# Performance work log

Hardware: AMD Instinct MI355X
Metric: run time of the kernel (lower is better)

## Reference

```python
import jax, jax.numpy as jnp
import numpy as np

D = 512
H = 8
DK = D // H
FF = 4 * D
EPS = 1e-5
NEG = -1.0e9


def _layernorm(x, g, b):
    mu = jnp.mean(x, axis=-1, keepdims=True)
    var = jnp.mean((x - mu) ** 2, axis=-1, keepdims=True)
    return (x - mu) * jax.lax.rsqrt(var + EPS) * g + b


def setup_inputs() -> dict:
    key = jax.random.key(0)
    ks = jax.random.split(key, 16)
    B, S = 4, 2048
    x = jax.random.normal(ks[0], (B, S, D), dtype=jnp.float32)
    # causal mask, broadcastable to [B, H, S, S]; mask==0 -> blocked
    mask = jnp.tril(jnp.ones((S, S), dtype=jnp.int32))[None, None]
    s = 1.0 / np.sqrt(D)
    sf = 1.0 / np.sqrt(FF)
    p = {
        "wq": jax.random.normal(ks[1], (D, D), jnp.float32) * s,
        "bq": jnp.zeros((D,), jnp.float32),
        "wk": jax.random.normal(ks[2], (D, D), jnp.float32) * s,
        "bk": jnp.zeros((D,), jnp.float32),
        "wv": jax.random.normal(ks[3], (D, D), jnp.float32) * s,
        "bv": jnp.zeros((D,), jnp.float32),
        "wo": jax.random.normal(ks[4], (D, D), jnp.float32) * s,
        "bo": jnp.zeros((D,), jnp.float32),
        "w1": jax.random.normal(ks[5], (D, FF), jnp.float32) * s,
        "b1": jnp.zeros((FF,), jnp.float32),
        "w2": jax.random.normal(ks[6], (FF, D), jnp.float32) * sf,
        "b2": jnp.zeros((D,), jnp.float32),
        "g1": jnp.ones((D,), jnp.float32),
        "be1": jnp.zeros((D,), jnp.float32),
        "g2": jnp.ones((D,), jnp.float32),
        "be2": jnp.zeros((D,), jnp.float32),
    }
    return {"x": x, "mask": mask, **p}


def reference(x, mask, wq, bq, wk, bk, wv, bv, wo, bo, w1, b1, w2, b2, g1, be1, g2, be2):
    B, S, _ = x.shape
    # projections -> [B, H, S, DK]
    q = (x @ wq + bq).reshape(B, S, H, DK).transpose(0, 2, 1, 3)
    k = (x @ wk + bk).reshape(B, S, H, DK).transpose(0, 2, 1, 3)
    v = (x @ wv + bv).reshape(B, S, H, DK).transpose(0, 2, 1, 3)
    scores = jnp.einsum("bhqd,bhkd->bhqk", q, k) / np.sqrt(DK)
    scores = jnp.where(mask == 0, NEG, scores)
    attn = jax.nn.softmax(scores, axis=-1)
    ctx = jnp.einsum("bhqk,bhkd->bhqd", attn, v)
    ctx = ctx.transpose(0, 2, 1, 3).reshape(B, S, D)
    attn_out = ctx @ wo + bo
    # dropout is inference-mode identity
    h = _layernorm(x + attn_out, g1, be1)
    ffn = jax.nn.relu(h @ w1 + b1) @ w2 + b2
    return _layernorm(h + ffn, g2, be2)
```

## Files before the change

kernel.cpp:

```cpp
#include <hip/hip_runtime.h>
#include <math.h>

#define D_   512
#define H_   8
#define DK_  64
#define FF_  2048
#define S_   2048
#define B_   4
#define M_   (B_*S_)
#define EPS_ 1e-5f
#define SCLQ 0.1803368801111f

typedef __attribute__((ext_vector_type(8))) short bf16x8;
typedef __attribute__((ext_vector_type(4))) float f32x4;
typedef __attribute__((ext_vector_type(4))) unsigned int u32x4;

__device__ inline unsigned short f2b(float f) {
    unsigned u = __builtin_bit_cast(unsigned, f);
    unsigned r = (u + 0x7FFFu + ((u >> 16) & 1u)) >> 16;
    return (unsigned short)r;
}
__device__ inline float b2f(unsigned short u) {
    return __builtin_bit_cast(float, (unsigned)u << 16);
}
__device__ inline unsigned packbf(float p0, float p1) {
    unsigned r;
    asm("v_cvt_pk_bf16_f32 %0, %1, %2" : "=v"(r) : "v"(p0), "v"(p1));
    return r;
}

__device__ __forceinline__ void async_cp16(const void* g, void* l) {
    __builtin_amdgcn_global_load_lds(
        (const __attribute__((address_space(1))) unsigned int*)g,
        (__attribute__((address_space(3))) unsigned int*)l, 16, 0, 0);
}

__global__ __launch_bounds__(256)
void prep_kernel(const float* __restrict__ x,
                 const float* __restrict__ wq, const float* __restrict__ wk,
                 const float* __restrict__ wv, const float* __restrict__ wo,
                 const float* __restrict__ bq, const float* __restrict__ bk,
                 const float* __restrict__ bv,
                 const float* __restrict__ w1, const float* __restrict__ w2,
                 unsigned short* __restrict__ xb, unsigned short* __restrict__ wqkvt,
                 unsigned short* __restrict__ wot, unsigned short* __restrict__ w1t,
                 unsigned short* __restrict__ w2t, float* __restrict__ bqkv)
{
    __shared__ float L[32][33];
    const int bid = blockIdx.x;
    const int tid = threadIdx.x;

    if (bid < 2048) {
        const int i = (bid * 256 + tid) * 8;
        const float4 a = *(const float4*)(x + i);
        const float4 b = *(const float4*)(x + i + 4);
        bf16x8 v;
        v[0] = (short)f2b(a.x); v[1] = (short)f2b(a.y);
        v[2] = (short)f2b(a.z); v[3] = (short)f2b(a.w);
        v[4] = (short)f2b(b.x); v[5] = (short)f2b(b.y);
        v[6] = (short)f2b(b.z); v[7] = (short)f2b(b.w);
        *(bf16x8*)(xb + i) = v;
        return;
    }

    const float* w; unsigned short* wt; int K, N, k0, n0; float scl = 1.f;
    if (bid < 3072) {
        const int z = (bid - 2048) >> 8;
        const int r = (bid - 2048) & 255;
        n0 = (r & 15) * 32; k0 = (r >> 4) * 32; K = 512; N = 512;
        w  = (z == 0) ? wq : (z == 1) ? wk : (z == 2) ? wv : wo;
        wt = (z < 3) ? (wqkvt + (size_t)z * 512 * 512) : wot;
        if (z == 0) scl = SCLQ;
        if (z < 3 && r == 0) {
            const float* bsrc = (z == 0) ? bq : (z == 1) ? bk : bv;
            const float bscl  = (z == 0) ? SCLQ : 1.f;
            bqkv[z * 512 + tid]       = bsrc[tid] * bscl;
            bqkv[z * 512 + 256 + tid] = bsrc[256 + tid] * bscl;
        }
    } else if (bid < 4096) {
        const int r = bid - 3072;
        n0 = (r & 63) * 32; k0 = (r >> 6) * 32; K = 512; N = 2048;
        w = w1; wt = w1t;
    } else {
        const int r = bid - 4096;
        n0 = (r & 15) * 32; k0 = (r >> 4) * 32; K = 2048; N = 512;
        w = w2; wt = w2t;
    }

    const int xx = tid & 31, y = tid >> 5;
#pragma unroll
    for (int i = 0; i < 4; i++)
        L[y + i * 8][xx] = w[(size_t)(k0 + y + i * 8) * N + n0 + xx] * scl;
    __syncthreads();
#pragma unroll
    for (int i = 0; i < 4; i++)
        wt[(size_t)(n0 + y + i * 8) * K + k0 + xx] = f2b(L[xx][y + i * 8]);
}

template<int WR, int WC, int MT, int NT, int BK, int OUTB, int RELU, int RESADD, int HASBIAS>
__global__ __launch_bounds__(256)
void gemm_bf16(const unsigned short* __restrict__ A, const unsigned short* __restrict__ Bt,
               const float* __restrict__ bias, const void* __restrict__ RES,
               void* __restrict__ Cv, int K, int lda, int ldb, int ldc)
{
    constexpr int BM  = WR * MT * 16;
    constexpr int BN  = WC * NT * 16;
    constexpr int CPR = BK / 8;
    constexpr int CA  = BM * BK / (256 * 8);
    constexpr int CB  = BN * BK / (256 * 8);
    __shared__ unsigned short As[2][BM * BK];
    __shared__ unsigned short Bs[2][BN * BK];

    const int tid  = threadIdx.x;
    const int lane = tid & 63;
    const int w    = tid >> 6;
    const int wr   = w / WC, wc = w % WC;
    const int quad = lane >> 4;
    const int l15  = lane & 15;
    const int n0   = blockIdx.x * BN;
    const int m0   = blockIdx.y * BM;

    f32x4 acc[MT][NT];
#pragma unroll
    for (int i = 0; i < MT; i++)
#pragma unroll
        for (int j = 0; j < NT; j++) acc[i][j] = (f32x4){0.f, 0.f, 0.f, 0.f};

    auto stage = [&](int k0, int bufi) {
#pragma unroll
        for (int i = 0; i < CA; i++) {
            const int c   = tid + i * 256;
            const int row = c / CPR;
            int l = c % CPR;
            if (BK == 64) l ^= (row & 7);
            async_cp16(&A[(size_t)(m0 + row) * lda + k0 + l * 8], &As[bufi][c * 8]);
        }
#pragma unroll
        for (int i = 0; i < CB; i++) {
            const int c   = tid + i * 256;
            const int row = c / CPR;
            int l = c % CPR;
            if (BK == 64) l ^= (row & 7);
            async_cp16(&Bt[(size_t)(n0 + row) * ldb + k0 + l * 8], &Bs[bufi][c * 8]);
        }
    };

    stage(0, 0);
    const int niter = K / BK;
    for (int ii = 0; ii < niter; ii++) {
        const int knext = (ii + 1 < niter) ? (ii + 1) * BK : 0;
        stage(knext, (ii + 1) & 1);
        __builtin_amdgcn_s_waitcnt(0x0f70 | (CA + CB));
        __builtin_amdgcn_s_barrier();

        const unsigned short* Ac = &As[ii & 1][0];
        const unsigned short* Bc = &Bs[ii & 1][0];
#pragma unroll
        for (int ks = 0; ks < BK / 32; ks++) {
            bf16x8 af[MT], bfr[NT];
#pragma unroll
            for (int t = 0; t < MT; t++) {
                const int r = wr * MT * 16 + t * 16 + l15;
                int ch = (ks << 2) | quad;
                if (BK == 64) ch ^= (r & 7);
                af[t] = *(const bf16x8*)&Ac[r * BK + ch * 8];
            }
#pragma unroll
            for (int t = 0; t < NT; t++) {
                const int r = wc * NT * 16 + t * 16 + l15;
                int ch = (ks << 2) | quad;
                if (BK == 64) ch ^= (r & 7);
                bfr[t] = *(const bf16x8*)&Bc[r * BK + ch * 8];
            }
#pragma unroll
            for (int mt = 0; mt < MT; mt++)
#pragma unroll
                for (int nt = 0; nt < NT; nt++)
                    acc[mt][nt] = __builtin_amdgcn_mfma_f32_16x16x32_bf16(
                        af[mt], bfr[nt], acc[mt][nt], 0, 0, 0);
        }
        __builtin_amdgcn_s_barrier();
    }

#pragma unroll
    for (int mt = 0; mt < MT; mt++) {
        const int rowb = m0 + wr * MT * 16 + mt * 16 + quad * 4;
#pragma unroll
        for (int nt = 0; nt < NT; nt++) {
            const int col = n0 + wc * NT * 16 + nt * 16 + l15;
            const float bv = HASBIAS ? bias[col] : 0.f;
#pragma unroll
            for (int r = 0; r < 4; r++) {
                const size_t idx = (size_t)(rowb + r) * ldc + col;
                float v = acc[mt][nt][r] + bv;
                if (RESADD == 1) v += ((const float*)RES)[idx];
                if (RESADD == 2) v += b2f(((const unsigned short*)RES)[idx]);
                if (RELU)   v = fmaxf(v, 0.f);
                if (OUTB) ((unsigned short*)Cv)[idx] = f2b(v);
                else      ((float*)Cv)[idx] = v;
            }
        }
    }
}

__global__ __launch_bounds__(256)
void vtrans(const unsigned short* __restrict__ qkv, unsigned short* __restrict__ vt)
{
    __shared__ unsigned short L[64][72];
    const int s0 = blockIdx.x * 64;
    const int bh = blockIdx.y;
    const int b  = bh >> 3, hh = bh & 7;
    const int tid = threadIdx.x;
    const unsigned short* src = qkv + (size_t)(b * S_) * 1536 + 1024 + hh * 64;
#pragma unroll
    for (int i = 0; i < 2; i++) {
        const int c = tid + i * 256;
        const int r = c >> 3, sub = (c & 7) * 8;
        *(bf16x8*)&L[r][sub] = *(const bf16x8*)(src + (size_t)(s0 + r) * 1536 + sub);
    }
    __syncthreads();
    const int dk = tid >> 2;
    const int sc = (tid & 3) * 16;
    bf16x8 t0, t1;
#pragma unroll
    for (int j = 0; j < 8; j++) t0[j] = (short)L[sc + j][dk];
#pragma unroll
    for (int j = 0; j < 8; j++) t1[j] = (short)L[sc + 8 + j][dk];
    unsigned short* dst = vt + (size_t)(bh * 64 + dk) * S_ + s0 + sc;
    *(bf16x8*)(dst)     = t0;
    *(bf16x8*)(dst + 8) = t1;
}

__global__ __launch_bounds__(256, 4)
void attn_mfma(const unsigned short* __restrict__ qkv,
               const unsigned short* __restrict__ vt,
               unsigned short* __restrict__ ctx)
{
    __shared__ unsigned short Ks[2][64 * 64];
    __shared__ unsigned short Vs[2][64 * 64];

    const int tid  = threadIdx.x;
    const int lane = tid & 63;
    const int w    = tid >> 6;
    const int quad = lane >> 4;
    const int l15  = lane & 15;
    const int bid  = blockIdx.x;
    const int g    = bid >> 5;
    const int qb   = (g < 8) ? 31 - g : (g < 16) ? g + 8 : (g < 24) ? 31 - g : g - 24;
    const int bh   = bid & 31;
    const int b    = bh >> 3, hh = bh & 7;
    const int kh   = w & 1;
    const int qh   = w >> 1;

    const unsigned short* qbase = qkv + (size_t)(b * S_) * 1536 + hh * 64;
    const unsigned short* kbase = qbase + 512;
    const unsigned short* vtb   = vt + (size_t)bh * 64 * S_;

    const int srcA  = 32 * (quad & 1) + l15;
    const int srcB  = srcA + 16;
    const bool selHi = (quad >> 1) != 0;

    bf16x8 ones;
#pragma unroll
    for (int j = 0; j < 8; j++) ones[j] = (short)0x3F80;

    auto stage = [&](int kb, int bufi) {
        unsigned short* kd = &Ks[bufi][0];
        unsigned short* vd = &Vs[bufi][0];
#pragma unroll
        for (int i = 0; i < 2; i++) {
            const int c = tid + i * 256;
            const int row = c >> 3;
            const int l = (c & 7) ^ (row & 7);
            async_cp16(kbase + (size_t)(kb * 64 + row) * 1536 + l * 8, kd + c * 8);
            async_cp16(vtb + (size_t)row * S_ + kb * 64 + l * 8, vd + c * 8);
        }
    };

    bf16x8 qf[2][2];
#pragma unroll
    for (int qt = 0; qt < 2; qt++) {
        const unsigned short* qr = qbase + (size_t)(qb * 64 + qh * 32 + qt * 16 + l15) * 1536;
        qf[qt][0] = *(const bf16x8*)(qr + quad * 8);
        qf[qt][1] = *(const bf16x8*)(qr + 32 + quad * 8);
    }

    f32x4 Oacc[2][5];
#pragma unroll
    for (int qt = 0; qt < 2; qt++)
#pragma unroll
        for (int i = 0; i < 5; i++) Oacc[qt][i] = (f32x4){0.f, 0.f, 0.f, 0.f};

    stage(0, 0);

    auto assemble2 = [&](const unsigned t0[2], const unsigned t1[2]) -> bf16x8 {
        const unsigned a0A = __shfl(t0[0], srcA, 64);
        const unsigned a1A = __shfl(t0[1], srcA, 64);
        const unsigned b0A = __shfl(t1[0], srcA, 64);
        const unsigned b1A = __shfl(t1[1], srcA, 64);
        const unsigned a0B = __shfl(t0[0], srcB, 64);
        const unsigned a1B = __shfl(t0[1], srcB, 64);
        const unsigned b0B = __shfl(t1[0], srcB, 64);
        const unsigned b1B = __shfl(t1[1], srcB, 64);
        u32x4 a;
        a[0] = selHi ? b0A : a0A;
        a[1] = selHi ? b1A : a1A;
        a[2] = selHi ? b0B : a0B;
        a[3] = selHi ? b1B : a1B;
        return __builtin_bit_cast(bf16x8, a);
    };

    const int physv = (kh * 4 + quad) ^ (l15 & 7);

    for (int kb = 0; kb < qb; kb++) {
        stage(kb + 1, (kb + 1) & 1);
        __builtin_amdgcn_s_waitcnt(0x0F74);
        __builtin_amdgcn_s_barrier();
        const unsigned short* Kc = &Ks[kb & 1][0];
        const unsigned short* Vc = &Vs[kb & 1][0];

        f32x4 st[2][2];
#pragma unroll
        for (int qt = 0; qt < 2; qt++)
#pragma unroll
            for (int kt = 0; kt < 2; kt++) st[qt][kt] = (f32x4){0.f, 0.f, 0.f, 0.f};
#pragma unroll
        for (int kc = 0; kc < 2; kc++) {
            const int phys = (kc * 4 + quad) ^ (l15 & 7);
            const bf16x8 kf0 = *(const bf16x8*)&Kc[(kh * 32 + l15) * 64 + phys * 8];
            const bf16x8 kf1 = *(const bf16x8*)&Kc[(kh * 32 + 16 + l15) * 64 + phys * 8];
#pragma unroll
            for (int qt = 0; qt < 2; qt++) {
                st[qt][0] = __builtin_amdgcn_mfma_f32_16x16x32_bf16(kf0, qf[qt][kc], st[qt][0], 0, 0, 0);
                st[qt][1] = __builtin_amdgcn_mfma_f32_16x16x32_bf16(kf1, qf[qt][kc], st[qt][1], 0, 0, 0);
            }
        }

        unsigned pk[2][2][2];
#pragma unroll
        for (int qt = 0; qt < 2; qt++)
#pragma unroll
            for (int kt = 0; kt < 2; kt++) {
                pk[qt][kt][0] = packbf(exp2f(st[qt][kt][0]), exp2f(st[qt][kt][1]));
                pk[qt][kt][1] = packbf(exp2f(st[qt][kt][2]), exp2f(st[qt][kt][3]));
            }

        bf16x8 vf[4];
#pragma unroll
        for (int nt = 0; nt < 4; nt++)
            vf[nt] = *(const bf16x8*)&Vc[(nt * 16 + l15) * 64 + physv * 8];
#pragma unroll
        for (int qt = 0; qt < 2; qt++) {
            const bf16x8 af = assemble2(pk[qt][0], pk[qt][1]);
#pragma unroll
            for (int nt = 0; nt < 4; nt++)
                Oacc[qt][nt] = __builtin_amdgcn_mfma_f32_16x16x32_bf16(af, vf[nt], Oacc[qt][nt], 0, 0, 0);
            Oacc[qt][4] = __builtin_amdgcn_mfma_f32_16x16x32_bf16(af, ones, Oacc[qt][4], 0, 0, 0);
        }
        __builtin_amdgcn_s_barrier();
    }

    {
        stage(0, (qb + 1) & 1);
        __builtin_amdgcn_s_waitcnt(0x0F74);
        __builtin_amdgcn_s_barrier();
        const unsigned short* Kc = &Ks[qb & 1][0];
        const unsigned short* Vc = &Vs[qb & 1][0];

        const bool skipDiag = (kh == 1 && qh == 0);
        const bool fullDiag = (kh == 0 && qh == 1);

        if (!skipDiag) {
            f32x4 st[2][2];
#pragma unroll
            for (int qt = 0; qt < 2; qt++)
#pragma unroll
                for (int kt = 0; kt < 2; kt++) st[qt][kt] = (f32x4){0.f, 0.f, 0.f, 0.f};
#pragma unroll
            for (int kc = 0; kc < 2; kc++) {
                const int phys = (kc * 4 + quad) ^ (l15 & 7);
                const bf16x8 kf0 = *(const bf16x8*)&Kc[(kh * 32 + l15) * 64 + phys * 8];
                const bf16x8 kf1 = *(const bf16x8*)&Kc[(kh * 32 + 16 + l15) * 64 + phys * 8];
#pragma unroll
                for (int qt = 0; qt < 2; qt++) {
                    st[qt][0] = __builtin_amdgcn_mfma_f32_16x16x32_bf16(kf0, qf[qt][kc], st[qt][0], 0, 0, 0);
                    st[qt][1] = __builtin_amdgcn_mfma_f32_16x16x32_bf16(kf1, qf[qt][kc], st[qt][1], 0, 0, 0);
                }
            }

            unsigned pk[2][2][2];
            if (fullDiag) {
#pragma unroll
                for (int qt = 0; qt < 2; qt++)
#pragma unroll
                    for (int kt = 0; kt < 2; kt++) {
                        pk[qt][kt][0] = packbf(exp2f(st[qt][kt][0]), exp2f(st[qt][kt][1]));
                        pk[qt][kt][1] = packbf(exp2f(st[qt][kt][2]), exp2f(st[qt][kt][3]));
                    }
            } else {
                float p[4];
#pragma unroll
                for (int r = 0; r < 4; r++)
                    p[r] = (quad * 4 + r > l15) ? 0.f : exp2f(st[0][0][r]);
                pk[0][0][0] = packbf(p[0], p[1]);
                pk[0][0][1] = packbf(p[2], p[3]);
                pk[0][1][0] = 0u; pk[0][1][1] = 0u;
                pk[1][0][0] = packbf(exp2f(st[1][0][0]), exp2f(st[1][0][1]));
                pk[1][0][1] = packbf(exp2f(st[1][0][2]), exp2f(st[1][0][3]));
#pragma unroll
                for (int r = 0; r < 4; r++)
                    p[r] = (quad * 4 + r > l15) ? 0.f : exp2f(st[1][1][r]);
                pk[1][1][0] = packbf(p[0], p[1]);
                pk[1][1][1] = packbf(p[2], p[3]);
            }

            bf16x8 vf[4];
#pragma unroll
            for (int nt = 0; nt < 4; nt++)
                vf[nt] = *(const bf16x8*)&Vc[(nt * 16 + l15) * 64 + physv * 8];
#pragma unroll
            for (int qt = 0; qt < 2; qt++) {
                const bf16x8 af = assemble2(pk[qt][0], pk[qt][1]);
#pragma unroll
                for (int nt = 0; nt < 4; nt++)
                    Oacc[qt][nt] = __builtin_amdgcn_mfma_f32_16x16x32_bf16(af, vf[nt], Oacc[qt][nt], 0, 0, 0);
                Oacc[qt][4] = __builtin_amdgcn_mfma_f32_16x16x32_bf16(af, ones, Oacc[qt][4], 0, 0, 0);
            }
        }
    }

    __syncthreads();
    float* red = (float*)&Ks[0][0];
    const int rbase = (qh * 64 + lane) * 44;
    if (kh) {
#pragma unroll
        for (int qt = 0; qt < 2; qt++)
#pragma unroll
            for (int i = 0; i < 5; i++)
                *(f32x4*)&red[rbase + (qt * 5 + i) * 4] = Oacc[qt][i];
    }
    __syncthreads();
    if (!kh) {
#pragma unroll
        for (int qt = 0; qt < 2; qt++)
#pragma unroll
            for (int i = 0; i < 5; i++)
                Oacc[qt][i] += *(const f32x4*)&red[rbase + (qt * 5 + i) * 4];

        unsigned short* cb = ctx + (size_t)(b * S_) * 512 + hh * 64;
#pragma unroll
        for (int qt = 0; qt < 2; qt++) {
            const int orow = qb * 64 + qh * 32 + qt * 16 + quad * 4;
#pragma unroll
            for (int r = 0; r < 4; r++) {
                const float inv = 1.f / Oacc[qt][4][r];
#pragma unroll
                for (int nt = 0; nt < 4; nt++)
                    cb[(size_t)(orow + r) * 512 + nt * 16 + l15] = f2b(Oacc[qt][nt][r] * inv);
            }
        }
    }
}

template<int WF, int WB>
__global__ __launch_bounds__(256)
void ln_kernel(const float* __restrict__ s, const float* __restrict__ g,
               const float* __restrict__ be, float* __restrict__ out,
               unsigned short* __restrict__ outb)
{
    const int wave = threadIdx.x >> 6;
    const int lane = threadIdx.x & 63;
    const int row  = blockIdx.x * 4 + wave;
    const float* ps = s + (size_t)row * D_;
    const int c0 = lane * 4;

    float v[8];
    {
        const float4 a0 = *(const float4*)(ps + c0);
        const float4 a1 = *(const float4*)(ps + c0 + 256);
        v[0] = a0.x; v[1] = a0.y; v[2] = a0.z; v[3] = a0.w;
        v[4] = a1.x; v[5] = a1.y; v[6] = a1.z; v[7] = a1.w;
    }

    float sum = 0.f;
#pragma unroll
    for (int i = 0; i < 8; i++) sum += v[i];
#pragma unroll
    for (int m = 1; m < 64; m <<= 1) sum += __shfl_xor(sum, m);
    const float mu = sum * (1.f / D_);

    float sq = 0.f;
#pragma unroll
    for (int i = 0; i < 8; i++) { const float d = v[i] - mu; sq += d * d; }
#pragma unroll
    for (int m = 1; m < 64; m <<= 1) sq += __shfl_xor(sq, m);
    const float rstd = rsqrtf(sq * (1.f / D_) + EPS_);

    const float4 g0 = *(const float4*)(g + c0);
    const float4 b0 = *(const float4*)(be + c0);
    const float4 g1 = *(const float4*)(g + c0 + 256);
    const float4 b1 = *(const float4*)(be + c0 + 256);

    float o[8];
    o[0] = (v[0] - mu) * rstd * g0.x + b0.x;
    o[1] = (v[1] - mu) * rstd * g0.y + b0.y;
    o[2] = (v[2] - mu) * rstd * g0.z + b0.z;
    o[3] = (v[3] - mu) * rstd * g0.w + b0.w;
    o[4] = (v[4] - mu) * rstd * g1.x + b1.x;
    o[5] = (v[5] - mu) * rstd * g1.y + b1.y;
    o[6] = (v[6] - mu) * rstd * g1.z + b1.z;
    o[7] = (v[7] - mu) * rstd * g1.w + b1.w;

    if (WF) {
        *(float4*)(out + (size_t)row * D_ + c0)       = *(float4*)&o[0];
        *(float4*)(out + (size_t)row * D_ + c0 + 256) = *(float4*)&o[4];
    }
    if (WB) {
        short4 vb0 = (short4){(short)f2b(o[0]), (short)f2b(o[1]), (short)f2b(o[2]), (short)f2b(o[3])};
        short4 vb1 = (short4){(short)f2b(o[4]), (short)f2b(o[5]), (short)f2b(o[6]), (short)f2b(o[7])};
        *(short4*)(outb + (size_t)row * D_ + c0)       = vb0;
        *(short4*)(outb + (size_t)row * D_ + c0 + 256) = vb1;
    }
}

extern "C" void kernel_launch(void* const* d_in, const int* in_sizes, int n_in,
                              void* d_out, int out_size, void* d_ws, size_t ws_size,
                              hipStream_t stream)
{
    const float* x  = (const float*)d_in[0];
    const float* wq = (const float*)d_in[2];
    const float* bq = (const float*)d_in[3];
    const float* wk = (const float*)d_in[4];
    const float* bk = (const float*)d_in[5];
    const float* wv = (const float*)d_in[6];
    const float* bv = (const float*)d_in[7];
    const float* wo = (const float*)d_in[8];
    const float* bo = (const float*)d_in[9];
    const float* w1 = (const float*)d_in[10];
    const float* b1 = (const float*)d_in[11];
    const float* w2 = (const float*)d_in[12];
    const float* b2 = (const float*)d_in[13];
    const float* g1 = (const float*)d_in[14];
    const float* be1= (const float*)d_in[15];
    const float* g2 = (const float*)d_in[16];
    const float* be2= (const float*)d_in[17];
    float* out = (float*)d_out;

    const size_t MB = 1048576;
    char* w8 = (char*)d_ws;
    unsigned short* wqkvt = (unsigned short*)(w8 + 0);
    unsigned short* wot   = (unsigned short*)(w8 + 1572864);
    unsigned short* w1t   = (unsigned short*)(w8 + 2097152);
    unsigned short* w2t   = (unsigned short*)(w8 + 4194304);
    float*          bqkv  = (float*)(w8 + 6291456);
    unsigned short* qkv   = (unsigned short*)(w8 + 8 * MB);
    unsigned short* ffn1b = qkv;
    unsigned short* xb    = (unsigned short*)(w8 + 40 * MB);
    unsigned short* ctx   = xb;
    unsigned short* vt    = (unsigned short*)(w8 + 48 * MB);
    unsigned short* hb    = vt;
    float*          pre   = (float*)(w8 + 56 * MB);

    const dim3 blk(256);

    prep_kernel<<<dim3(5120), blk, 0, stream>>>(
        x, wq, wk, wv, wo, bq, bk, bv, w1, w2, xb, wqkvt, wot, w1t, w2t, bqkv);

    gemm_bf16<2,2,4,4,32,1,0,0,1><<<dim3(12, 64), blk, 0, stream>>>(
        xb, wqkvt, bqkv, nullptr, qkv, 512, 512, 512, 1536);

    vtrans<<<dim3(32, 32), blk, 0, stream>>>(qkv, vt);

    attn_mfma<<<dim3(1024), blk, 0, stream>>>(qkv, vt, ctx);

    gemm_bf16<2,2,2,4,64,0,0,1,1><<<dim3(4, 128), blk, 0, stream>>>(
        ctx, wot, bo, x, pre, 512, 512, 512, 512);

    ln_kernel<1,1><<<dim3(M_ / 4), blk, 0, stream>>>(pre, g1, be1, pre, hb);

    gemm_bf16<2,2,4,4,32,1,1,0,1><<<dim3(16, 64), blk, 0, stream>>>(
        hb, w1t, b1, nullptr, ffn1b, 512, 512, 512, 2048);

    gemm_bf16<2,2,2,4,64,0,0,1,1><<<dim3(4, 128), blk, 0, stream>>>(
        ffn1b, w2t, b2, pre, pre, 2048, 2048, 2048, 512);

    ln_kernel<1,0><<<dim3(M_ / 4), blk, 0, stream>>>(pre, g2, be2, out, nullptr);
}
```

Baseline: 274.9 us.

## Split attention block across 8 waves with one 16-row Q tile each

Doubles the attention block from 256 to 512 threads so each of 8 waves owns a single 16-row query tile instead of two, halving per-wave accumulators and register use. K/V staging now issues one async copy per thread per tile with the waitcnt adjusted to match, and the diagonal-block masking is rewritten for the four query sub-tiles. The aim is more waves in flight to hide latency in the MFMA/exp loop, at the cost of K/V fragment loads from LDS being shared across fewer query rows per wave and barriers spanning more waves.

```diff
diff --git a/kernel.cpp b/kernel.cpp
--- a/kernel.cpp
+++ b/kernel.cpp
@@ -231,13 +231,12 @@
     *(bf16x8*)(dst + 8) = t1;
 }
 
-__global__ __launch_bounds__(256, 4)
+__global__ __launch_bounds__(512, 8)
 void attn_mfma(const unsigned short* __restrict__ qkv,
                const unsigned short* __restrict__ vt,
                unsigned short* __restrict__ ctx)
 {
-    __shared__ unsigned short Ks[2][64 * 64];
-    __shared__ unsigned short Vs[2][64 * 64];
+    __shared__ unsigned short S[4][64 * 64];
 
     const int tid  = threadIdx.x;
     const int lane = tid & 63;
@@ -250,7 +249,7 @@
     const int bh   = bid & 31;
     const int b    = bh >> 3, hh = bh & 7;
     const int kh   = w & 1;
-    const int qh   = w >> 1;
+    const int qq   = w >> 1;
 
     const unsigned short* qbase = qkv + (size_t)(b * S_) * 1536 + hh * 64;
     const unsigned short* kbase = qbase + 512;
@@ -265,31 +264,23 @@
     for (int j = 0; j < 8; j++) ones[j] = (short)0x3F80;
 
     auto stage = [&](int kb, int bufi) {
-        unsigned short* kd = &Ks[bufi][0];
-        unsigned short* vd = &Vs[bufi][0];
-#pragma unroll
-        for (int i = 0; i < 2; i++) {
-            const int c = tid + i * 256;
-            const int row = c >> 3;
-            const int l = (c & 7) ^ (row & 7);
-            async_cp16(kbase + (size_t)(kb * 64 + row) * 1536 + l * 8, kd + c * 8);
-            async_cp16(vtb + (size_t)row * S_ + kb * 64 + l * 8, vd + c * 8);
-        }
+        const int c   = tid;
+        const int row = c >> 3;
+        const int l   = (c & 7) ^ (row & 7);
+        async_cp16(kbase + (size_t)(kb * 64 + row) * 1536 + l * 8, &S[bufi][c * 8]);
+        async_cp16(vtb + (size_t)row * S_ + kb * 64 + l * 8, &S[2 + bufi][c * 8]);
     };
 
-    bf16x8 qf[2][2];
-#pragma unroll
-    for (int qt = 0; qt < 2; qt++) {
-        const unsigned short* qr = qbase + (size_t)(qb * 64 + qh * 32 + qt * 16 + l15) * 1536;
-        qf[qt][0] = *(const bf16x8*)(qr + quad * 8);
-        qf[qt][1] = *(const bf16x8*)(qr + 32 + quad * 8);
-    }
-
-    f32x4 Oacc[2][5];
-#pragma unroll
-    for (int qt = 0; qt < 2; qt++)
-#pragma unroll
-        for (int i = 0; i < 5; i++) Oacc[qt][i] = (f32x4){0.f, 0.f, 0.f, 0.f};
+    bf16x8 qf[2];
+    {
+        const unsigned short* qr = qbase + (size_t)(qb * 64 + qq * 16 + l15) * 1536;
+        qf[0] = *(const bf16x8*)(qr + quad * 8);
+        qf[1] = *(const bf16x8*)(qr + 32 + quad * 8);
+    }
+
+    f32x4 Oacc[5];
+#pragma unroll
+    for (int i = 0; i < 5; i++) Oacc[i] = (f32x4){0.f, 0.f, 0.f, 0.f};
 
     stage(0, 0);
 
@@ -314,150 +305,123 @@
 
     for (int kb = 0; kb < qb; kb++) {
         stage(kb + 1, (kb + 1) & 1);
-        __builtin_amdgcn_s_waitcnt(0x0F74);
+        __builtin_amdgcn_s_waitcnt(0x0F72);
         __builtin_amdgcn_s_barrier();
-        const unsigned short* Kc = &Ks[kb & 1][0];
-        const unsigned short* Vc = &Vs[kb & 1][0];
-
-        f32x4 st[2][2];
-#pragma unroll
-        for (int qt = 0; qt < 2; qt++)
-#pragma unroll
-            for (int kt = 0; kt < 2; kt++) st[qt][kt] = (f32x4){0.f, 0.f, 0.f, 0.f};
+        const unsigned short* Kc = &S[kb & 1][0];
+        const unsigned short* Vc = &S[2 + (kb & 1)][0];
+
+        f32x4 st[2];
+        st[0] = (f32x4){0.f, 0.f, 0.f, 0.f};
+        st[1] = (f32x4){0.f, 0.f, 0.f, 0.f};
 #pragma unroll
         for (int kc = 0; kc < 2; kc++) {
             const int phys = (kc * 4 + quad) ^ (l15 & 7);
             const bf16x8 kf0 = *(const bf16x8*)&Kc[(kh * 32 + l15) * 64 + phys * 8];
             const bf16x8 kf1 = *(const bf16x8*)&Kc[(kh * 32 + 16 + l15) * 64 + phys * 8];
-#pragma unroll
-            for (int qt = 0; qt < 2; qt++) {
-                st[qt][0] = __builtin_amdgcn_mfma_f32_16x16x32_bf16(kf0, qf[qt][kc], st[qt][0], 0, 0, 0);
-                st[qt][1] = __builtin_amdgcn_mfma_f32_16x16x32_bf16(kf1, qf[qt][kc], st[qt][1], 0, 0, 0);
-            }
-        }
-
-        unsigned pk[2][2][2];
-#pragma unroll
-        for (int qt = 0; qt < 2; qt++)
-#pragma unroll
-            for (int kt = 0; kt < 2; kt++) {
-                pk[qt][kt][0] = packbf(exp2f(st[qt][kt][0]), exp2f(st[qt][kt][1]));
-                pk[qt][kt][1] = packbf(exp2f(st[qt][kt][2]), exp2f(st[qt][kt][3]));
-            }
+            st[0] = __builtin_amdgcn_mfma_f32_16x16x32_bf16(kf0, qf[kc], st[0], 0, 0, 0);
+            st[1] = __builtin_amdgcn_mfma_f32_16x16x32_bf16(kf1, qf[kc], st[1], 0, 0, 0);
+        }
+
+        unsigned pk[2][2];
+#pragma unroll
+        for (int kt = 0; kt < 2; kt++) {
+            pk[kt][0] = packbf(exp2f(st[kt][0]), exp2f(st[kt][1]));
+            pk[kt][1] = packbf(exp2f(st[kt][2]), exp2f(st[kt][3]));
+        }
 
         bf16x8 vf[4];
 #pragma unroll
         for (int nt = 0; nt < 4; nt++)
             vf[nt] = *(const bf16x8*)&Vc[(nt * 16 + l15) * 64 + physv * 8];
-#pragma unroll
-        for (int qt = 0; qt < 2; qt++) {
-            const bf16x8 af = assemble2(pk[qt][0], pk[qt][1]);
-#pragma unroll
-            for (int nt = 0; nt < 4; nt++)
-                Oacc[qt][nt] = __builtin_amdgcn_mfma_f32_16x16x32_bf16(af, vf[nt], Oacc[qt][nt], 0, 0, 0);
-            Oacc[qt][4] = __builtin_amdgcn_mfma_f32_16x16x32_bf16(af, ones, Oacc[qt][4], 0, 0, 0);
-        }
+        const bf16x8 af = assemble2(pk[0], pk[1]);
+#pragma unroll
+        for (int nt = 0; nt < 4; nt++)
+            Oacc[nt] = __builtin_amdgcn_mfma_f32_16x16x32_bf16(af, vf[nt], Oacc[nt], 0, 0, 0);
+        Oacc[4] = __builtin_amdgcn_mfma_f32_16x16x32_bf16(af, ones, Oacc[4], 0, 0, 0);
         __builtin_amdgcn_s_barrier();
     }
 
     {
         stage(0, (qb + 1) & 1);
-        __builtin_amdgcn_s_waitcnt(0x0F74);
+        __builtin_amdgcn_s_waitcnt(0x0F72);
         __builtin_amdgcn_s_barrier();
-        const unsigned short* Kc = &Ks[qb & 1][0];
-        const unsigned short* Vc = &Vs[qb & 1][0];
-
-        const bool skipDiag = (kh == 1 && qh == 0);
-        const bool fullDiag = (kh == 0 && qh == 1);
-
-        if (!skipDiag) {
-            f32x4 st[2][2];
-#pragma unroll
-            for (int qt = 0; qt < 2; qt++)
-#pragma unroll
-                for (int kt = 0; kt < 2; kt++) st[qt][kt] = (f32x4){0.f, 0.f, 0.f, 0.f};
+        const unsigned short* Kc = &S[qb & 1][0];
+        const unsigned short* Vc = &S[2 + (qb & 1)][0];
+
+        const int d = qq - 2 * kh;
+        if (d >= 0) {
+            f32x4 st[2];
+            st[0] = (f32x4){0.f, 0.f, 0.f, 0.f};
+            st[1] = (f32x4){0.f, 0.f, 0.f, 0.f};
 #pragma unroll
             for (int kc = 0; kc < 2; kc++) {
                 const int phys = (kc * 4 + quad) ^ (l15 & 7);
                 const bf16x8 kf0 = *(const bf16x8*)&Kc[(kh * 32 + l15) * 64 + phys * 8];
                 const bf16x8 kf1 = *(const bf16x8*)&Kc[(kh * 32 + 16 + l15) * 64 + phys * 8];
-#pragma unroll
-                for (int qt = 0; qt < 2; qt++) {
-                    st[qt][0] = __builtin_amdgcn_mfma_f32_16x16x32_bf16(kf0, qf[qt][kc], st[qt][0], 0, 0, 0);
-                    st[qt][1] = __builtin_amdgcn_mfma_f32_16x16x32_bf16(kf1, qf[qt][kc], st[qt][1], 0, 0, 0);
+                st[0] = __builtin_amdgcn_mfma_f32_16x16x32_bf16(kf0, qf[kc], st[0], 0, 0, 0);
+                st[1] = __builtin_amdgcn_mfma_f32_16x16x32_bf16(kf1, qf[kc], st[1], 0, 0, 0);
+            }
+
+            unsigned pk[2][2];
+            if (d >= 2) {
+#pragma unroll
+                for (int kt = 0; kt < 2; kt++) {
+                    pk[kt][0] = packbf(exp2f(st[kt][0]), exp2f(st[kt][1]));
+                    pk[kt][1] = packbf(exp2f(st[kt][2]), exp2f(st[kt][3]));
                 }
-            }
-
-            unsigned pk[2][2][2];
-            if (fullDiag) {
-#pragma unroll
-                for (int qt = 0; qt < 2; qt++)
-#pragma unroll
-                    for (int kt = 0; kt < 2; kt++) {
-                        pk[qt][kt][0] = packbf(exp2f(st[qt][kt][0]), exp2f(st[qt][kt][1]));
-                        pk[qt][kt][1] = packbf(exp2f(st[qt][kt][2]), exp2f(st[qt][kt][3]));
-                    }
+            } else if (d == 1) {
+                pk[0][0] = packbf(exp2f(st[0][0]), exp2f(st[0][1]));
+                pk[0][1] = packbf(exp2f(st[0][2]), exp2f(st[0][3]));
+                float p[4];
+#pragma unroll
+                for (int r = 0; r < 4; r++)
+                    p[r] = (quad * 4 + r > l15) ? 0.f : exp2f(st[1][r]);
+                pk[1][0] = packbf(p[0], p[1]);
+                pk[1][1] = packbf(p[2], p[3]);
             } else {
                 float p[4];
 #pragma unroll
                 for (int r = 0; r < 4; r++)
-                    p[r] = (quad * 4 + r > l15) ? 0.f : exp2f(st[0][0][r]);
-                pk[0][0][0] = packbf(p[0], p[1]);
-                pk[0][0][1] = packbf(p[2], p[3]);
-                pk[0][1][0] = 0u; pk[0][1][1] = 0u;
-                pk[1][0][0] = packbf(exp2f(st[1][0][0]), exp2f(st[1][0][1]));
-                pk[1][0][1] = packbf(exp2f(st[1][0][2]), exp2f(st[1][0][3]));
-#pragma unroll
-                for (int r = 0; r < 4; r++)
-                    p[r] = (quad * 4 + r > l15) ? 0.f : exp2f(st[1][1][r]);
-                pk[1][1][0] = packbf(p[0], p[1]);
-                pk[1][1][1] = packbf(p[2], p[3]);
+                    p[r] = (quad * 4 + r > l15) ? 0.f : exp2f(st[0][r]);
+                pk[0][0] = packbf(p[0], p[1]);
+                pk[0][1] = packbf(p[2], p[3]);
+                pk[1][0] = 0u; pk[1][1] = 0u;
             }
 
             bf16x8 vf[4];
 #pragma unroll
             for (int nt = 0; nt < 4; nt++)
                 vf[nt] = *(const bf16x8*)&Vc[(nt * 16 + l15) * 64 + physv * 8];
-#pragma unroll
-            for (int qt = 0; qt < 2; qt++) {
-                const bf16x8 af = assemble2(pk[qt][0], pk[qt][1]);
-#pragma unroll
-                for (int nt = 0; nt < 4; nt++)
-                    Oacc[qt][nt] = __builtin_amdgcn_mfma_f32_16x16x32_bf16(af, vf[nt], Oacc[qt][nt], 0, 0, 0);
-                Oacc[qt][4] = __builtin_amdgcn_mfma_f32_16x16x32_bf16(af, ones, Oacc[qt][4], 0, 0, 0);
-            }
+            const bf16x8 af = assemble2(pk[0], pk[1]);
+#pragma unroll
+            for (int nt = 0; nt < 4; nt++)
+                Oacc[nt] = __builtin_amdgcn_mfma_f32_16x16x32_bf16(af, vf[nt], Oacc[nt], 0, 0, 0);
+            Oacc[4] = __builtin_amdgcn_mfma_f32_16x16x32_bf16(af, ones, Oacc[4], 0, 0, 0);
         }
     }
 
     __syncthreads();
-    float* red = (float*)&Ks[0][0];
-    const int rbase = (qh * 64 + lane) * 44;
+    float* red = (float*)&S[0][0];
+    const int rbase = (qq * 64 + lane) * 20;
     if (kh) {
 #pragma unroll
-        for (int qt = 0; qt < 2; qt++)
-#pragma unroll
-            for (int i = 0; i < 5; i++)
-                *(f32x4*)&red[rbase + (qt * 5 + i) * 4] = Oacc[qt][i];
+        for (int i = 0; i < 5; i++)
+            *(f32x4*)&red[rbase + i * 4] = Oacc[i];
     }
     __syncthreads();
     if (!kh) {
 #pragma unroll
-        for (int qt = 0; qt < 2; qt++)
-#pragma unroll
-            for (int i = 0; i < 5; i++)
-                Oacc[qt][i] += *(const f32x4*)&red[rbase + (qt * 5 + i) * 4];
+        for (int i = 0; i < 5; i++)
+            Oacc[i] += *(const f32x4*)&red[rbase + i * 4];
 
         unsigned short* cb = ctx + (size_t)(b * S_) * 512 + hh * 64;
-#pragma unroll
-        for (int qt = 0; qt < 2; qt++) {
-            const int orow = qb * 64 + qh * 32 + qt * 16 + quad * 4;
-#pragma unroll
-            for (int r = 0; r < 4; r++) {
-                const float inv = 1.f / Oacc[qt][4][r];
-#pragma unroll
-                for (int nt = 0; nt < 4; nt++)
-                    cb[(size_t)(orow + r) * 512 + nt * 16 + l15] = f2b(Oacc[qt][nt][r] * inv);
-            }
+        const int orow = qb * 64 + qq * 16 + quad * 4;
+#pragma unroll
+        for (int r = 0; r < 4; r++) {
+            const float inv = 1.f / Oacc[4][r];
+#pragma unroll
+            for (int nt = 0; nt < 4; nt++)
+                cb[(size_t)(orow + r) * 512 + nt * 16 + l15] = f2b(Oacc[nt][r] * inv);
         }
     }
 }
@@ -571,7 +535,7 @@
 
     vtrans<<<dim3(32, 32), blk, 0, stream>>>(qkv, vt);
 
-    attn_mfma<<<dim3(1024), blk, 0, stream>>>(qkv, vt, ctx);
+    attn_mfma<<<dim3(1024), dim3(512), 0, stream>>>(qkv, vt, ctx);
 
     gemm_bf16<2,2,2,4,64,0,0,1,1><<<dim3(4, 128), blk, 0, stream>>>(
         ctx, wot, bo, x, pre, 512, 512, 512, 512);
```

New measurement: 275.5 us. Within noise of the previous version (+0.2%).
